# Performance work log

Measured on AMD Instinct MI355X. Metric: run time of the kernel, lower is better.

The kernel has to match this reference:

```python
import jax, jax.numpy as jnp
import numpy as np

B, S, H = 2, 2048, 2048
NH, NKV = 16, 4
DH = H // NH            # 128
I = 4 * H               # 8192
EPS = 1e-6


def rms_norm(x, w, eps=EPS):
    xf = x.astype(jnp.float32)
    var = jnp.mean(xf * xf, axis=-1, keepdims=True)
    return (w * (xf * jax.lax.rsqrt(var + eps))).astype(x.dtype)


def rotate_half(x):
    x1, x2 = jnp.split(x, 2, axis=-1)
    return jnp.concatenate([-x2, x1], axis=-1)


def setup_inputs() -> dict:
    key = jax.random.key(0)
    ks = jax.random.split(key, 12)
    hidden_states = jax.random.normal(ks[0], (B, S, H), jnp.float32)
    # rotary cos/sin over head_dim, standard RoPE table
    inv_freq = 1.0 / (10000.0 ** (np.arange(0, DH, 2, dtype=np.float32) / DH))
    t = np.arange(S, dtype=np.float32)
    freqs = np.einsum('i,j->ij', t, inv_freq)          # [S, DH/2]
    emb = np.concatenate([freqs, freqs], axis=-1)      # [S, DH]
    cos = jnp.broadcast_to(jnp.asarray(np.cos(emb))[None], (B, S, DH))
    sin = jnp.broadcast_to(jnp.asarray(np.sin(emb))[None], (B, S, DH))
    sd = lambda fan_in: 1.0 / np.sqrt(fan_in)
    return {
        'hidden_states': hidden_states,
        'cos': cos, 'sin': sin,
        'wq': jax.random.normal(ks[1], (H, NH * DH), jnp.float32) * sd(H),
        'wk': jax.random.normal(ks[2], (H, NKV * DH), jnp.float32) * sd(H),
        'wv': jax.random.normal(ks[3], (H, NKV * DH), jnp.float32) * sd(H),
        'wo': jax.random.normal(ks[4], (NH * DH, H), jnp.float32) * sd(H),
        'q_norm_w': jnp.ones((DH,), jnp.float32),
        'k_norm_w': jnp.ones((DH,), jnp.float32),
        'attn_norm_w': jnp.ones((H,), jnp.float32),
        'mlp_norm_w': jnp.ones((H,), jnp.float32),
        'w_gate': jax.random.normal(ks[5], (H, I), jnp.float32) * sd(H),
        'w_up': jax.random.normal(ks[6], (H, I), jnp.float32) * sd(H),
        'w_down': jax.random.normal(ks[7], (I, H), jnp.float32) * sd(I),
    }


def reference(hidden_states, cos, sin, wq, wk, wv, wo,
              q_norm_w, k_norm_w, attn_norm_w, mlp_norm_w,
              w_gate, w_up, w_down):
    b, s, _ = hidden_states.shape
    groups = NH // NKV
    scaling = DH ** -0.5

    # ---- attention sub-block ----
    residual = hidden_states
    x = rms_norm(hidden_states, attn_norm_w)

    q = (x @ wq).reshape(b, s, NH, DH)
    k = (x @ wk).reshape(b, s, NKV, DH)
    v = (x @ wv).reshape(b, s, NKV, DH)

    # per-head RMSNorm on head_dim (QK-norm)
    q = rms_norm(q, q_norm_w)
    k = rms_norm(k, k_norm_w)

    q = q.transpose(0, 2, 1, 3)  # [b, NH, s, DH]
    k = k.transpose(0, 2, 1, 3)  # [b, NKV, s, DH]
    v = v.transpose(0, 2, 1, 3)

    c = cos[:, None]  # [b, 1, s, DH]
    sn = sin[:, None]
    q = q * c + rotate_half(q) * sn
    k = k * c + rotate_half(k) * sn

    # GQA: fold query heads into [b, NKV, groups, s, DH]; avoid repeat_kv copy
    qg = q.reshape(b, NKV, groups, s, DH)
    scores = jnp.einsum('bkgqd,bkjd->bkgqj', qg, k) * scaling
    probs = jax.nn.softmax(scores.astype(jnp.float32), axis=-1).astype(hidden_states.dtype)
    attn = jnp.einsum('bkgqj,bkjd->bkgqd', probs, v)  # [b, NKV, groups, s, DH]
    attn = attn.reshape(b, NH, s, DH).transpose(0, 2, 1, 3).reshape(b, s, NH * DH)
    hidden_states = residual + attn @ wo

    # ---- SwiGLU MLP sub-block ----
    residual = hidden_states
    x = rms_norm(hidden_states, mlp_norm_w)
    h = jax.nn.silu(x @ w_gate) * (x @ w_up)
    hidden_states = residual + h @ w_down
    return hidden_states
```

## Files before the change

### kernel.cpp

```cpp
#include <hip/hip_runtime.h>
#include <stdint.h>

#define B_ 2
#define S_ 2048
#define H_ 2048
#define NH_ 16
#define NKV_ 4
#define DH_ 128
#define M_ (B_*S_)

typedef unsigned short u16;
typedef __attribute__((ext_vector_type(8))) short short8;
typedef __attribute__((ext_vector_type(4))) float floatx4;

__device__ __forceinline__ float b2f(u16 h) {
  union { unsigned int u; float f; } v; v.u = ((unsigned int)h) << 16; return v.f;
}
__device__ __forceinline__ u16 f2b(float f) {
  union { float f; unsigned int u; } v; v.f = f;
  unsigned int u = v.u;
  unsigned int r = (u + 0x7FFFu + ((u >> 16) & 1u)) >> 16;
  return (u16)r;
}
__device__ __forceinline__ floatx4 mfma16(short8 a, short8 b, floatx4 c) {
  return __builtin_amdgcn_mfma_f32_16x16x32_bf16(a, b, c, 0, 0, 0);
}
__device__ __forceinline__ void gld16(const u16* g, u16* l) {
  __builtin_amdgcn_global_load_lds(
      (const __attribute__((address_space(1))) unsigned int*)g,
      (__attribute__((address_space(3))) unsigned int*)l, 16, 0, 0);
}

__global__ __launch_bounds__(256) void transpose_kernel(const float* __restrict__ Bm,
                                                        u16* __restrict__ BT,
                                                        int K, int N) {
  __shared__ u16 sl[64][68];
  int t = threadIdx.x;
  int n0 = blockIdx.x * 64, k0 = blockIdx.y * 64;
#pragma unroll
  for (int p = 0; p < 4; ++p) {
    int kk = p * 16 + (t >> 4);
    int nn = (t & 15) * 4;
    float4 v = *(const float4*)&Bm[(size_t)(k0 + kk) * N + n0 + nn];
    sl[kk][nn + 0] = f2b(v.x); sl[kk][nn + 1] = f2b(v.y);
    sl[kk][nn + 2] = f2b(v.z); sl[kk][nn + 3] = f2b(v.w);
  }
  __syncthreads();
#pragma unroll
  for (int p = 0; p < 2; ++p) {
    int nn = p * 32 + (t >> 3);
    int kc = (t & 7) * 8;
    u16 ov[8];
#pragma unroll
    for (int j = 0; j < 8; ++j) ov[j] = sl[kc + j][nn];
    *(uint4*)&BT[(size_t)(n0 + nn) * K + k0 + kc] = *(uint4*)ov;
  }
}

__global__ __launch_bounds__(256) void rmsnorm_kernel(const float* __restrict__ x,
                                                      const float* __restrict__ w,
                                                      u16* __restrict__ o) {
  int row = blockIdx.x;
  int tid = threadIdx.x;
  const float* xr = x + (size_t)row * H_ + tid * 8;
  float4 a = *(const float4*)xr;
  float4 b = *(const float4*)(xr + 4);
  float xf[8] = {a.x, a.y, a.z, a.w, b.x, b.y, b.z, b.w};
  float ss = 0.f;
#pragma unroll
  for (int i = 0; i < 8; ++i) ss += xf[i] * xf[i];
#pragma unroll
  for (int m = 32; m >= 1; m >>= 1) ss += __shfl_xor(ss, m, 64);
  __shared__ float red[4];
  if ((tid & 63) == 0) red[tid >> 6] = ss;
  __syncthreads();
  float tot = red[0] + red[1] + red[2] + red[3];
  float scale = rsqrtf(tot / (float)H_ + 1e-6f);
  const float* wr = w + tid * 8;
  float4 wa = *(const float4*)wr;
  float4 wb = *(const float4*)(wr + 4);
  float wf[8] = {wa.x, wa.y, wa.z, wa.w, wb.x, wb.y, wb.z, wb.w};
  u16 ov[8];
#pragma unroll
  for (int i = 0; i < 8; ++i) ov[i] = f2b(xf[i] * scale * wf[i]);
  *(uint4*)&o[(size_t)row * H_ + tid * 8] = *(uint4*)ov;
}

template <int OUTF>
__global__ __launch_bounds__(256) void gemm_t(const u16* __restrict__ A,
                                              const u16* __restrict__ BT,
                                              void* __restrict__ Cv,
                                              const float* __restrict__ Res,
                                              int M, int N, int K) {
  __shared__ u16 sa[128 * 32];
  __shared__ u16 sb[128 * 32];
  const int tid = threadIdx.x;
  const int lane = tid & 63, w = tid >> 6;
  const int q4 = lane >> 4, l15 = lane & 15;
  const int wr = (w >> 1) * 64, wc = (w & 1) * 64;
  const int m0 = blockIdx.y * 128, n0 = blockIdx.x * 128;
  const int srow = lane >> 2, skc = (lane & 3) * 8;
  const int c0 = w * 2;
  floatx4 acc[4][4] = {};
  const u16* aG0 = A  + (size_t)(m0 + (c0 + 0) * 16 + srow) * K + skc;
  const u16* aG1 = A  + (size_t)(m0 + (c0 + 1) * 16 + srow) * K + skc;
  const u16* bG0 = BT + (size_t)(n0 + (c0 + 0) * 16 + srow) * K + skc;
  const u16* bG1 = BT + (size_t)(n0 + (c0 + 1) * 16 + srow) * K + skc;
  u16* aL0 = sa + (c0 + 0) * 512;
  u16* aL1 = sa + (c0 + 1) * 512;
  u16* bL0 = sb + (c0 + 0) * 512;
  u16* bL1 = sb + (c0 + 1) * 512;

  for (int k0 = 0; k0 < K; k0 += 32) {
    __syncthreads();
    gld16(aG0 + k0, aL0);
    gld16(aG1 + k0, aL1);
    gld16(bG0 + k0, bL0);
    gld16(bG1 + k0, bL1);
    __syncthreads();
    short8 af[4], bf[4];
#pragma unroll
    for (int i = 0; i < 4; ++i)
      af[i] = *(const short8*)&sa[(wr + i * 16 + l15) * 32 + q4 * 8];
#pragma unroll
    for (int j = 0; j < 4; ++j)
      bf[j] = *(const short8*)&sb[(wc + j * 16 + l15) * 32 + q4 * 8];
#pragma unroll
    for (int i = 0; i < 4; ++i)
#pragma unroll
      for (int j = 0; j < 4; ++j)
        acc[i][j] = mfma16(af[i], bf[j], acc[i][j]);
  }
#pragma unroll
  for (int i = 0; i < 4; ++i)
#pragma unroll
    for (int j = 0; j < 4; ++j)
#pragma unroll
      for (int r = 0; r < 4; ++r) {
        int row = m0 + wr + i * 16 + q4 * 4 + r;
        int col = n0 + wc + j * 16 + l15;
        float v = acc[i][j][r];
        if (OUTF) {
          if (Res) v += Res[(size_t)row * N + col];
          ((float*)Cv)[(size_t)row * N + col] = v;
        } else {
          ((u16*)Cv)[(size_t)row * N + col] = f2b(v);
        }
      }
}

__global__ __launch_bounds__(256) void gateup_kernel(const u16* __restrict__ A,
                                                     const u16* __restrict__ GT,
                                                     const u16* __restrict__ UT,
                                                     u16* __restrict__ O,
                                                     int M, int N, int K) {
  __shared__ u16 sa[128 * 32];
  __shared__ u16 sg[64 * 32];
  __shared__ u16 su[64 * 32];
  const int tid = threadIdx.x;
  const int lane = tid & 63, w = tid >> 6;
  const int q4 = lane >> 4, l15 = lane & 15;
  const int wr = (w >> 1) * 64, wc = (w & 1) * 32;
  const int m0 = blockIdx.y * 128, n0 = blockIdx.x * 64;
  const int srow = lane >> 2, skc = (lane & 3) * 8;
  const int c0 = w * 2;
  floatx4 accg[4][2] = {};
  floatx4 accu[4][2] = {};
  const u16* aG0 = A  + (size_t)(m0 + (c0 + 0) * 16 + srow) * K + skc;
  const u16* aG1 = A  + (size_t)(m0 + (c0 + 1) * 16 + srow) * K + skc;
  const u16* gG  = GT + (size_t)(n0 + w * 16 + srow) * K + skc;
  const u16* uG  = UT + (size_t)(n0 + w * 16 + srow) * K + skc;
  u16* aL0 = sa + (c0 + 0) * 512;
  u16* aL1 = sa + (c0 + 1) * 512;
  u16* gL  = sg + w * 512;
  u16* uL  = su + w * 512;

  for (int k0 = 0; k0 < K; k0 += 32) {
    __syncthreads();
    gld16(aG0 + k0, aL0);
    gld16(aG1 + k0, aL1);
    gld16(gG + k0, gL);
    gld16(uG + k0, uL);
    __syncthreads();
    short8 af[4], gf[2], uf[2];
#pragma unroll
    for (int i = 0; i < 4; ++i)
      af[i] = *(const short8*)&sa[(wr + i * 16 + l15) * 32 + q4 * 8];
#pragma unroll
    for (int j = 0; j < 2; ++j) {
      gf[j] = *(const short8*)&sg[(wc + j * 16 + l15) * 32 + q4 * 8];
      uf[j] = *(const short8*)&su[(wc + j * 16 + l15) * 32 + q4 * 8];
    }
#pragma unroll
    for (int i = 0; i < 4; ++i)
#pragma unroll
      for (int j = 0; j < 2; ++j) {
        accg[i][j] = mfma16(af[i], gf[j], accg[i][j]);
        accu[i][j] = mfma16(af[i], uf[j], accu[i][j]);
      }
  }
#pragma unroll
  for (int i = 0; i < 4; ++i)
#pragma unroll
    for (int j = 0; j < 2; ++j)
#pragma unroll
      for (int r = 0; r < 4; ++r) {
        int row = m0 + wr + i * 16 + q4 * 4 + r;
        int col = n0 + wc + j * 16 + l15;
        float g = accg[i][j][r];
        float u = accu[i][j][r];
        float s = g / (1.f + __expf(-g));
        O[(size_t)row * N + col] = f2b(s * u);
      }
}

__global__ __launch_bounds__(256) void qknorm_rope_kernel(u16* __restrict__ x,
                                                          const float* __restrict__ nw,
                                                          const float* __restrict__ cs,
                                                          const float* __restrict__ sn,
                                                          int nheads, int rowStride) {
  int lane = threadIdx.x & 63;
  int w = threadIdx.x >> 6;
  int gw = blockIdx.x * 4 + w;
  int t = gw / nheads, h = gw % nheads;
  u16* xp = x + (size_t)t * rowStride + h * DH_;
  float x0 = b2f(xp[lane]), x1 = b2f(xp[lane + 64]);
  float ss = x0 * x0 + x1 * x1;
#pragma unroll
  for (int m = 32; m >= 1; m >>= 1) ss += __shfl_xor(ss, m, 64);
  float scale = rsqrtf(ss / 128.f + 1e-6f);
  float n0 = x0 * scale * nw[lane];
  float n1 = x1 * scale * nw[lane + 64];
  const float* cp = cs + (size_t)t * DH_;
  const float* sp = sn + (size_t)t * DH_;
  float c0 = cp[lane], c1 = cp[lane + 64];
  float s0 = sp[lane], s1 = sp[lane + 64];
  xp[lane]      = f2b(n0 * c0 - n1 * s0);
  xp[lane + 64] = f2b(n1 * c1 + n0 * s1);
}

__global__ __launch_bounds__(256) void attn_kernel(const u16* __restrict__ qb,
                                                   const u16* __restrict__ kb,
                                                   const u16* __restrict__ vb,
                                                   u16* __restrict__ ob) {
  __shared__ u16 q_lds[64][136];
  __shared__ u16 k_lds[64][136];
  __shared__ u16 vt_lds[128][72];
  __shared__ u16 p_lds[4][16][72];
  const int QSTR = NH_ * DH_ + NKV_ * DH_ * 2;
  int tid = threadIdx.x;
  int lane = tid & 63, w = tid >> 6;
  int q4 = lane >> 4, l15 = lane & 15;
  int qt = blockIdx.x & 31;
  int h = (blockIdx.x >> 5) & 15;
  int b = blockIdx.x >> 9;
  int kvh = h >> 2;
  int srow = tid >> 2;
  int sd0 = (tid & 3) * 32;
  const float scaling = 0.08838834764831845f;

  {
    const u16* qsrc = qb + (size_t)(b * S_ + qt * 64 + srow) * QSTR + h * DH_;
#pragma unroll
    for (int ii = 0; ii < 4; ++ii) {
      int d = sd0 + ii * 8;
      *(uint4*)&q_lds[srow][d] = *(const uint4*)&qsrc[d];
    }
  }

  float m_i[4], l_i[4];
  floatx4 o_acc[8] = {};
#pragma unroll
  for (int r = 0; r < 4; ++r) { m_i[r] = -1e30f; l_i[r] = 0.f; }

  for (int c = 0; c < S_ / 64; ++c) {
    int j0 = c * 64;
    __syncthreads();
    const u16* ksrc = kb + (size_t)(b * S_ + j0 + srow) * QSTR + kvh * DH_;
    const u16* vsrc = vb + (size_t)(b * S_ + j0 + srow) * QSTR + kvh * DH_;
#pragma unroll
    for (int ii = 0; ii < 4; ++ii) {
      int d = sd0 + ii * 8;
      *(uint4*)&k_lds[srow][d] = *(const uint4*)&ksrc[d];
      uint4 vv = *(const uint4*)&vsrc[d];
      const u16* ve = (const u16*)&vv;
#pragma unroll
      for (int e = 0; e < 8; ++e) vt_lds[d + e][srow] = ve[e];
    }
    __syncthreads();

    floatx4 sc[4];
#pragma unroll
    for (int js = 0; js < 4; ++js) {
      floatx4 a = {};
#pragma unroll
      for (int kk = 0; kk < 4; ++kk) {
        short8 qa  = *(const short8*)&q_lds[w * 16 + l15][kk * 32 + q4 * 8];
        short8 kbf = *(const short8*)&k_lds[js * 16 + l15][kk * 32 + q4 * 8];
        a = mfma16(qa, kbf, a);
      }
      sc[js] = a;
    }
    float mx[4];
#pragma unroll
    for (int r = 0; r < 4; ++r)
      mx[r] = fmaxf(fmaxf(sc[0][r], sc[1][r]), fmaxf(sc[2][r], sc[3][r])) * scaling;
#pragma unroll
    for (int m = 8; m >= 1; m >>= 1)
#pragma unroll
      for (int r = 0; r < 4; ++r) mx[r] = fmaxf(mx[r], __shfl_xor(mx[r], m, 64));
    float alpha[4], rs[4];
#pragma unroll
    for (int r = 0; r < 4; ++r) {
      float mnew = fmaxf(m_i[r], mx[r]);
      alpha[r] = __expf(m_i[r] - mnew);
      m_i[r] = mnew;
      rs[r] = 0.f;
    }
#pragma unroll
    for (int js = 0; js < 4; ++js)
#pragma unroll
      for (int r = 0; r < 4; ++r) {
        float p = __expf(sc[js][r] * scaling - m_i[r]);
        rs[r] += p;
        p_lds[w][q4 * 4 + r][js * 16 + l15] = f2b(p);
      }
#pragma unroll
    for (int m = 8; m >= 1; m >>= 1)
#pragma unroll
      for (int r = 0; r < 4; ++r) rs[r] += __shfl_xor(rs[r], m, 64);
#pragma unroll
    for (int r = 0; r < 4; ++r) l_i[r] = l_i[r] * alpha[r] + rs[r];
#pragma unroll
    for (int d2 = 0; d2 < 8; ++d2)
#pragma unroll
      for (int r = 0; r < 4; ++r) o_acc[d2][r] *= alpha[r];
    __syncthreads();
#pragma unroll
    for (int d2 = 0; d2 < 8; ++d2) {
#pragma unroll
      for (int kk = 0; kk < 2; ++kk) {
        short8 pa  = *(const short8*)&p_lds[w][l15][kk * 32 + q4 * 8];
        short8 vbf = *(const short8*)&vt_lds[d2 * 16 + l15][kk * 32 + q4 * 8];
        o_acc[d2] = mfma16(pa, vbf, o_acc[d2]);
      }
    }
  }
#pragma unroll
  for (int d2 = 0; d2 < 8; ++d2)
#pragma unroll
    for (int r = 0; r < 4; ++r) {
      int row = qt * 64 + w * 16 + q4 * 4 + r;
      float val = o_acc[d2][r] / l_i[r];
      ob[(size_t)(b * S_ + row) * (NH_ * DH_) + h * DH_ + d2 * 16 + l15] = f2b(val);
    }
}

extern "C" void kernel_launch(void* const* d_in, const int* in_sizes, int n_in,
                              void* d_out, int out_size, void* d_ws, size_t ws_size,
                              hipStream_t stream) {
  const float* hs   = (const float*)d_in[0];
  const float* cosb = (const float*)d_in[1];
  const float* sinb = (const float*)d_in[2];
  const float* wq   = (const float*)d_in[3];
  const float* wk   = (const float*)d_in[4];
  const float* wv   = (const float*)d_in[5];
  const float* wo   = (const float*)d_in[6];
  const float* qnw  = (const float*)d_in[7];
  const float* knw  = (const float*)d_in[8];
  const float* anw  = (const float*)d_in[9];
  const float* mnw  = (const float*)d_in[10];
  const float* wg   = (const float*)d_in[11];
  const float* wu   = (const float*)d_in[12];
  const float* wd   = (const float*)d_in[13];
  float* out = (float*)d_out;
  u16* ws  = (u16*)d_ws;

  u16* wqkvT = ws;
  u16* woT   = ws + 6291456;
  u16* wgT   = ws + 10485760;
  u16* wuT   = ws + 27262976;
  u16* wdT   = ws + 44040192;
  u16* xn    = ws + 60817408;
  u16* qkv   = ws + 69206016;
  float* h1  = (float*)(ws + 81788928);
  u16* hbuf  = ws + 98566144;

  transpose_kernel<<<dim3(2048/64, 2048/64), 256, 0, stream>>>(wq, wqkvT, 2048, 2048);
  transpose_kernel<<<dim3(512/64,  2048/64), 256, 0, stream>>>(wk, wqkvT + (size_t)2048*2048, 2048, 512);
  transpose_kernel<<<dim3(512/64,  2048/64), 256, 0, stream>>>(wv, wqkvT + (size_t)2560*2048, 2048, 512);
  transpose_kernel<<<dim3(2048/64, 2048/64), 256, 0, stream>>>(wo, woT, 2048, 2048);
  transpose_kernel<<<dim3(8192/64, 2048/64), 256, 0, stream>>>(wg, wgT, 2048, 8192);
  transpose_kernel<<<dim3(8192/64, 2048/64), 256, 0, stream>>>(wu, wuT, 2048, 8192);
  transpose_kernel<<<dim3(2048/64, 8192/64), 256, 0, stream>>>(wd, wdT, 8192, 2048);

  rmsnorm_kernel<<<M_, 256, 0, stream>>>(hs, anw, xn);
  gemm_t<0><<<dim3(3072/128, M_/128), 256, 0, stream>>>(xn, wqkvT, qkv, nullptr, M_, 3072, 2048);
  qknorm_rope_kernel<<<M_ * NH_  / 4, 256, 0, stream>>>(qkv,        qnw, cosb, sinb, NH_,  3072);
  qknorm_rope_kernel<<<M_ * NKV_ / 4, 256, 0, stream>>>(qkv + 2048, knw, cosb, sinb, NKV_, 3072);
  attn_kernel<<<B_ * NH_ * (S_ / 64), 256, 0, stream>>>(qkv, qkv + 2048, qkv + 2560, xn);
  gemm_t<1><<<dim3(2048/128, M_/128), 256, 0, stream>>>(xn, woT, h1, hs, M_, 2048, 2048);
  u16* x2 = qkv;
  rmsnorm_kernel<<<M_, 256, 0, stream>>>(h1, mnw, x2);
  gateup_kernel<<<dim3(8192/64, M_/128), 256, 0, stream>>>(x2, wgT, wuT, hbuf, M_, 8192, 2048);
  gemm_t<1><<<dim3(2048/128, M_/128), 256, 0, stream>>>(hbuf, wdT, out, h1, M_, 2048, 8192);
}
```

Before: 1.280 ms.

## Replace GEMMs with 4-stage pipelined 256-row tile kernel with swizzled LDS

The simple single-buffered GEMM and fused gate/up kernel are replaced by one templated GEMM. It uses 512 threads, 256xBN tiles and a 4-deep LDS ring buffer with vmcnt-based waits, so global loads overlap MFMA work. LDS columns are XOR-swizzled to cut bank conflicts, and s_setprio is raised around the MFMA blocks. The gate/up fusion is split into two passes: up is written first as bf16, then the gate GEMM reads it back in its epilogue to apply SiLU. This adds an extra read and write of the intermediate plus a rounding of up to bf16 before the multiply. LDS use is much larger, which may limit occupancy.

Result: slower. 1.405 ms (+9.8%).

```diff
diff --git a/kernel.cpp b/kernel.cpp
--- a/kernel.cpp
+++ b/kernel.cpp
@@ -86,132 +86,102 @@
   *(uint4*)&o[(size_t)row * H_ + tid * 8] = *(uint4*)ov;
 }
 
-template <int OUTF>
-__global__ __launch_bounds__(256) void gemm_t(const u16* __restrict__ A,
+template <int BN, int OUTF>
+__global__ __launch_bounds__(512) void gemm_p(const u16* __restrict__ A,
                                               const u16* __restrict__ BT,
                                               void* __restrict__ Cv,
                                               const float* __restrict__ Res,
                                               int M, int N, int K) {
-  __shared__ u16 sa[128 * 32];
-  __shared__ u16 sb[128 * 32];
+  constexpr int WN    = (BN == 256) ? 4 : 2;
+  constexpr int WROWS = (BN == 256) ? 128 : 64;
+  constexpr int AFRAG = WROWS / 16;
+  constexpr int IPT   = 2 + BN / 128;
+  __shared__ __align__(16) u16 sa[4][256 * 32];
+  __shared__ __align__(16) u16 sb[4][BN * 32];
   const int tid = threadIdx.x;
   const int lane = tid & 63, w = tid >> 6;
   const int q4 = lane >> 4, l15 = lane & 15;
-  const int wr = (w >> 1) * 64, wc = (w & 1) * 64;
-  const int m0 = blockIdx.y * 128, n0 = blockIdx.x * 128;
-  const int srow = lane >> 2, skc = (lane & 3) * 8;
-  const int c0 = w * 2;
-  floatx4 acc[4][4] = {};
-  const u16* aG0 = A  + (size_t)(m0 + (c0 + 0) * 16 + srow) * K + skc;
-  const u16* aG1 = A  + (size_t)(m0 + (c0 + 1) * 16 + srow) * K + skc;
-  const u16* bG0 = BT + (size_t)(n0 + (c0 + 0) * 16 + srow) * K + skc;
-  const u16* bG1 = BT + (size_t)(n0 + (c0 + 1) * 16 + srow) * K + skc;
-  u16* aL0 = sa + (c0 + 0) * 512;
-  u16* aL1 = sa + (c0 + 1) * 512;
-  u16* bL0 = sb + (c0 + 0) * 512;
-  u16* bL1 = sb + (c0 + 1) * 512;
-
-  for (int k0 = 0; k0 < K; k0 += 32) {
-    __syncthreads();
-    gld16(aG0 + k0, aL0);
-    gld16(aG1 + k0, aL1);
-    gld16(bG0 + k0, bL0);
-    gld16(bG1 + k0, bL1);
-    __syncthreads();
-    short8 af[4], bf[4];
-#pragma unroll
-    for (int i = 0; i < 4; ++i)
-      af[i] = *(const short8*)&sa[(wr + i * 16 + l15) * 32 + q4 * 8];
+  const int wm = w / WN, wn = w % WN;
+  const int m0 = blockIdx.y * 256, n0 = blockIdx.x * BN;
+  const int srow = tid >> 2;
+  const int scb  = (tid & 3) ^ ((tid >> 3) & 3);
+  const u16* aS = A  + (size_t)(m0 + srow) * K + scb * 8;
+  const u16* bS = BT + (size_t)(n0 + srow) * K + scb * 8;
+  const int lOff = w * 512;
+  const int colSwz = (q4 ^ ((l15 >> 1) & 3)) * 8;
+  const int arow0 = wm * WROWS + l15;
+  const int brow0 = wn * 64 + l15;
+  const int NT = K / 32;
+  floatx4 acc[AFRAG][4] = {};
+
+  auto stage = [&](int tt) {
+    const int bb = tt & 3;
+    const int ko = tt * 32;
+    gld16(aS + ko,                   &sa[bb][lOff]);
+    gld16(aS + (size_t)128 * K + ko, &sa[bb][4096 + lOff]);
+    gld16(bS + ko,                   &sb[bb][lOff]);
+    if constexpr (BN == 256)
+      gld16(bS + (size_t)128 * K + ko, &sb[bb][4096 + lOff]);
+  };
+
+  stage(0); stage(1); stage(2);
+  for (int t = 0; t < NT; ++t) {
+    const u16* sab = sa[t & 3];
+    const u16* sbb = sb[t & 3];
+    const int left = NT - 1 - t;
+    if (left >= 2) {
+      asm volatile("s_waitcnt vmcnt(%0)" :: "n"(2 * IPT) : "memory");
+    } else if (left == 1) {
+      asm volatile("s_waitcnt vmcnt(%0)" :: "n"(IPT) : "memory");
+    } else {
+      asm volatile("s_waitcnt vmcnt(0)" ::: "memory");
+    }
+    __builtin_amdgcn_s_barrier();
+    asm volatile("" ::: "memory");
+    if (t + 3 < NT) stage(t + 3);
+    short8 bfr[4];
 #pragma unroll
     for (int j = 0; j < 4; ++j)
-      bf[j] = *(const short8*)&sb[(wc + j * 16 + l15) * 32 + q4 * 8];
-#pragma unroll
-    for (int i = 0; i < 4; ++i)
-#pragma unroll
-      for (int j = 0; j < 4; ++j)
-        acc[i][j] = mfma16(af[i], bf[j], acc[i][j]);
-  }
-#pragma unroll
-  for (int i = 0; i < 4; ++i)
-#pragma unroll
-    for (int j = 0; j < 4; ++j)
+      bfr[j] = *(const short8*)&sbb[(brow0 + j * 16) * 32 + colSwz];
+#pragma unroll
+    for (int ih = 0; ih < AFRAG / 4; ++ih) {
+      short8 afr[4];
+#pragma unroll
+      for (int i2 = 0; i2 < 4; ++i2)
+        afr[i2] = *(const short8*)&sab[(arow0 + (ih * 4 + i2) * 16) * 32 + colSwz];
+      __builtin_amdgcn_s_setprio(1);
+#pragma unroll
+      for (int i2 = 0; i2 < 4; ++i2)
+#pragma unroll
+        for (int j = 0; j < 4; ++j)
+          acc[ih * 4 + i2][j] = mfma16(afr[i2], bfr[j], acc[ih * 4 + i2][j]);
+      __builtin_amdgcn_s_setprio(0);
+    }
+  }
+
+#pragma unroll
+  for (int i = 0; i < AFRAG; ++i)
+#pragma unroll
+    for (int j = 0; j < 4; ++j) {
+      const int row0 = m0 + wm * WROWS + i * 16 + q4 * 4;
+      const int col  = n0 + wn * 64 + j * 16 + l15;
 #pragma unroll
       for (int r = 0; r < 4; ++r) {
-        int row = m0 + wr + i * 16 + q4 * 4 + r;
-        int col = n0 + wc + j * 16 + l15;
+        const size_t idx = (size_t)(row0 + r) * N + col;
         float v = acc[i][j][r];
-        if (OUTF) {
-          if (Res) v += Res[(size_t)row * N + col];
-          ((float*)Cv)[(size_t)row * N + col] = v;
+        if constexpr (OUTF == 1) {
+          if (Res) v += Res[idx];
+          ((float*)Cv)[idx] = v;
+        } else if constexpr (OUTF == 2) {
+          u16* O = (u16*)Cv;
+          float u = b2f(O[idx]);
+          float s = v / (1.f + __expf(-v));
+          O[idx] = f2b(s * u);
         } else {
-          ((u16*)Cv)[(size_t)row * N + col] = f2b(v);
+          ((u16*)Cv)[idx] = f2b(v);
         }
       }
-}
-
-__global__ __launch_bounds__(256) void gateup_kernel(const u16* __restrict__ A,
-                                                     const u16* __restrict__ GT,
-                                                     const u16* __restrict__ UT,
-                                                     u16* __restrict__ O,
-                                                     int M, int N, int K) {
-  __shared__ u16 sa[128 * 32];
-  __shared__ u16 sg[64 * 32];
-  __shared__ u16 su[64 * 32];
-  const int tid = threadIdx.x;
-  const int lane = tid & 63, w = tid >> 6;
-  const int q4 = lane >> 4, l15 = lane & 15;
-  const int wr = (w >> 1) * 64, wc = (w & 1) * 32;
-  const int m0 = blockIdx.y * 128, n0 = blockIdx.x * 64;
-  const int srow = lane >> 2, skc = (lane & 3) * 8;
-  const int c0 = w * 2;
-  floatx4 accg[4][2] = {};
-  floatx4 accu[4][2] = {};
-  const u16* aG0 = A  + (size_t)(m0 + (c0 + 0) * 16 + srow) * K + skc;
-  const u16* aG1 = A  + (size_t)(m0 + (c0 + 1) * 16 + srow) * K + skc;
-  const u16* gG  = GT + (size_t)(n0 + w * 16 + srow) * K + skc;
-  const u16* uG  = UT + (size_t)(n0 + w * 16 + srow) * K + skc;
-  u16* aL0 = sa + (c0 + 0) * 512;
-  u16* aL1 = sa + (c0 + 1) * 512;
-  u16* gL  = sg + w * 512;
-  u16* uL  = su + w * 512;
-
-  for (int k0 = 0; k0 < K; k0 += 32) {
-    __syncthreads();
-    gld16(aG0 + k0, aL0);
-    gld16(aG1 + k0, aL1);
-    gld16(gG + k0, gL);
-    gld16(uG + k0, uL);
-    __syncthreads();
-    short8 af[4], gf[2], uf[2];
-#pragma unroll
-    for (int i = 0; i < 4; ++i)
-      af[i] = *(const short8*)&sa[(wr + i * 16 + l15) * 32 + q4 * 8];
-#pragma unroll
-    for (int j = 0; j < 2; ++j) {
-      gf[j] = *(const short8*)&sg[(wc + j * 16 + l15) * 32 + q4 * 8];
-      uf[j] = *(const short8*)&su[(wc + j * 16 + l15) * 32 + q4 * 8];
-    }
-#pragma unroll
-    for (int i = 0; i < 4; ++i)
-#pragma unroll
-      for (int j = 0; j < 2; ++j) {
-        accg[i][j] = mfma16(af[i], gf[j], accg[i][j]);
-        accu[i][j] = mfma16(af[i], uf[j], accu[i][j]);
-      }
-  }
-#pragma unroll
-  for (int i = 0; i < 4; ++i)
-#pragma unroll
-    for (int j = 0; j < 2; ++j)
-#pragma unroll
-      for (int r = 0; r < 4; ++r) {
-        int row = m0 + wr + i * 16 + q4 * 4 + r;
-        int col = n0 + wc + j * 16 + l15;
-        float g = accg[i][j][r];
-        float u = accu[i][j][r];
-        float s = g / (1.f + __expf(-g));
-        O[(size_t)row * N + col] = f2b(s * u);
-      }
+    }
 }
 
 __global__ __launch_bounds__(256) void qknorm_rope_kernel(u16* __restrict__ x,
@@ -395,13 +365,14 @@
   transpose_kernel<<<dim3(2048/64, 8192/64), 256, 0, stream>>>(wd, wdT, 8192, 2048);
 
   rmsnorm_kernel<<<M_, 256, 0, stream>>>(hs, anw, xn);
-  gemm_t<0><<<dim3(3072/128, M_/128), 256, 0, stream>>>(xn, wqkvT, qkv, nullptr, M_, 3072, 2048);
+  gemm_p<256,0><<<dim3(3072/256, M_/256), 512, 0, stream>>>(xn, wqkvT, qkv, nullptr, M_, 3072, 2048);
   qknorm_rope_kernel<<<M_ * NH_  / 4, 256, 0, stream>>>(qkv,        qnw, cosb, sinb, NH_,  3072);
   qknorm_rope_kernel<<<M_ * NKV_ / 4, 256, 0, stream>>>(qkv + 2048, knw, cosb, sinb, NKV_, 3072);
   attn_kernel<<<B_ * NH_ * (S_ / 64), 256, 0, stream>>>(qkv, qkv + 2048, qkv + 2560, xn);
-  gemm_t<1><<<dim3(2048/128, M_/128), 256, 0, stream>>>(xn, woT, h1, hs, M_, 2048, 2048);
+  gemm_p<128,1><<<dim3(2048/128, M_/256), 512, 0, stream>>>(xn, woT, h1, hs, M_, 2048, 2048);
   u16* x2 = qkv;
   rmsnorm_kernel<<<M_, 256, 0, stream>>>(h1, mnw, x2);
-  gateup_kernel<<<dim3(8192/64, M_/128), 256, 0, stream>>>(x2, wgT, wuT, hbuf, M_, 8192, 2048);
-  gemm_t<1><<<dim3(2048/128, M_/128), 256, 0, stream>>>(hbuf, wdT, out, h1, M_, 2048, 8192);
-}
+  gemm_p<256,0><<<dim3(8192/256, M_/256), 512, 0, stream>>>(x2, wuT, hbuf, nullptr, M_, 8192, 2048);
+  gemm_p<256,2><<<dim3(8192/256, M_/256), 512, 0, stream>>>(x2, wgT, hbuf, nullptr, M_, 8192, 2048);
+  gemm_p<128,1><<<dim3(2048/128, M_/256), 512, 0, stream>>>(hbuf, wdT, out, h1, M_, 2048, 8192);
+}
```

## Add 256x256 pipelined GEMM with interleaved gate/up weights for QKV and MLP

Applied to the files above, without the earlier changes.

Adds a new 512-thread GEMM kernel with 256x256 tiles, a double-buffered LDS pipeline using direct global-to-LDS loads, XOR-swizzled LDS layout, explicit barriers and waitcnts, priority hints, and XCD-aware block remapping. Gate and up weights are transposed into one interleaved matrix in 128-column blocks, so a single GEMM produces both, and the SwiGLU is applied in the epilogue by exchanging the up half through LDS. The new kernel replaces both the QKV projection and the old gate/up kernel. It relies on hand-placed synchronization and register pressure at occupancy 2, and the up values are rounded to bf16 before the multiply.

Measured after the change: 1.244 ms. -2.8%, faster.

```diff
diff --git a/kernel.cpp b/kernel.cpp
--- a/kernel.cpp
+++ b/kernel.cpp
@@ -31,9 +31,16 @@
       (__attribute__((address_space(3))) unsigned int*)l, 16, 0, 0);
 }
 
+#define BAR()    asm volatile("s_barrier" ::: "memory")
+#define LGKM0()  asm volatile("s_waitcnt lgkmcnt(0)" ::: "memory")
+#define VMC(n)   asm volatile("s_waitcnt vmcnt(" #n ")" ::: "memory")
+#define SCHEDB() __builtin_amdgcn_sched_barrier(0)
+#define PRIO1()  __builtin_amdgcn_s_setprio(1)
+#define PRIO0()  __builtin_amdgcn_s_setprio(0)
+
 __global__ __launch_bounds__(256) void transpose_kernel(const float* __restrict__ Bm,
                                                         u16* __restrict__ BT,
-                                                        int K, int N) {
+                                                        int K, int N, int ileave) {
   __shared__ u16 sl[64][68];
   int t = threadIdx.x;
   int n0 = blockIdx.x * 64, k0 = blockIdx.y * 64;
@@ -53,7 +60,10 @@
     u16 ov[8];
 #pragma unroll
     for (int j = 0; j < 8; ++j) ov[j] = sl[kc + j][nn];
-    *(uint4*)&BT[(size_t)(n0 + nn) * K + k0 + kc] = *(uint4*)ov;
+    int n = n0 + nn;
+    int n_out = n;
+    if (ileave) n_out = ((n >> 7) << 8) + ((ileave == 2) ? 128 : 0) + (n & 127);
+    *(uint4*)&BT[(size_t)n_out * K + k0 + kc] = *(uint4*)ov;
   }
 }
 
@@ -149,69 +159,189 @@
       }
 }
 
-__global__ __launch_bounds__(256) void gateup_kernel(const u16* __restrict__ A,
-                                                     const u16* __restrict__ GT,
-                                                     const u16* __restrict__ UT,
-                                                     u16* __restrict__ O,
-                                                     int M, int N, int K) {
-  __shared__ u16 sa[128 * 32];
-  __shared__ u16 sg[64 * 32];
-  __shared__ u16 su[64 * 32];
+template <int OUTF>
+__global__ __launch_bounds__(512, 2) void gemm8(const u16* __restrict__ A,
+                                                const u16* __restrict__ BT,
+                                                void* __restrict__ Cv,
+                                                int M, int N, int K,
+                                                int gm, int ldO) {
+  __shared__ u16 sA[2][2][8192];
+  __shared__ u16 sB[2][2][8192];
   const int tid = threadIdx.x;
   const int lane = tid & 63, w = tid >> 6;
   const int q4 = lane >> 4, l15 = lane & 15;
-  const int wr = (w >> 1) * 64, wc = (w & 1) * 32;
-  const int m0 = blockIdx.y * 128, n0 = blockIdx.x * 64;
-  const int srow = lane >> 2, skc = (lane & 3) * 8;
-  const int c0 = w * 2;
-  floatx4 accg[4][2] = {};
-  floatx4 accu[4][2] = {};
-  const u16* aG0 = A  + (size_t)(m0 + (c0 + 0) * 16 + srow) * K + skc;
-  const u16* aG1 = A  + (size_t)(m0 + (c0 + 1) * 16 + srow) * K + skc;
-  const u16* gG  = GT + (size_t)(n0 + w * 16 + srow) * K + skc;
-  const u16* uG  = UT + (size_t)(n0 + w * 16 + srow) * K + skc;
-  u16* aL0 = sa + (c0 + 0) * 512;
-  u16* aL1 = sa + (c0 + 1) * 512;
-  u16* gL  = sg + w * 512;
-  u16* uL  = su + w * 512;
-
-  for (int k0 = 0; k0 < K; k0 += 32) {
-    __syncthreads();
-    gld16(aG0 + k0, aL0);
-    gld16(aG1 + k0, aL1);
-    gld16(gG + k0, gL);
-    gld16(uG + k0, uL);
-    __syncthreads();
-    short8 af[4], gf[2], uf[2];
+  const int wm = w >> 2, wn = w & 3;
+  const int nwg = gridDim.x;
+  const int qx = nwg >> 3, rx = nwg & 7;
+  const int xcd = blockIdx.x & 7, idxx = blockIdx.x >> 3;
+  const int wgid = (xcd < rx ? xcd * (qx + 1) : rx * (qx + 1) + (xcd - rx) * qx) + idxx;
+  const int m0 = (wgid % gm) * 256, n0 = (wgid / gm) * 256;
+
+  const int sr = tid >> 3;
+  const int sblk = ((tid & 7) ^ (sr & 7)) << 3;
+  const u16* aS = A  + (size_t)(m0 + sr) * K + sblk;
+  const u16* bS = BT + (size_t)(n0 + sr) * K + sblk;
+  const size_t K64 = (size_t)K << 6;
+  const int wofs = w * 512;
+
+  const int cA  = (q4 ^ (l15 & 7)) << 3;
+  const int bh  = wn >> 1;
+  const int bb  = (wn & 1) * 64;
+  const int NT  = K >> 6;
+
+  floatx4 acc[8][4] = {};
+
+  auto stA = [&](int c, int k0) {
+    const u16* s0 = aS + k0;
+    gld16(s0,            &sA[c][0][wofs]);
+    gld16(s0 + K64,      &sA[c][0][4096 + wofs]);
+    gld16(s0 + 2 * K64,  &sA[c][1][wofs]);
+    gld16(s0 + 3 * K64,  &sA[c][1][4096 + wofs]);
+  };
+  auto stB = [&](int c, int k0) {
+    const u16* s0 = bS + k0;
+    gld16(s0,            &sB[c][0][wofs]);
+    gld16(s0 + K64,      &sB[c][0][4096 + wofs]);
+    gld16(s0 + 2 * K64,  &sB[c][1][wofs]);
+    gld16(s0 + 3 * K64,  &sB[c][1][4096 + wofs]);
+  };
+
+  stB(0, 0); stA(0, 0);
+  stB(1, 64); stA(1, 64);
+  VMC(8);
+  BAR();
+
+  short8 aR[4][2], bR[4][2];
+#pragma unroll 1
+  for (int t = 0; t < NT; ++t) {
+    const int c = t & 1;
+    const u16* aH = &sA[c][wm][0];
+    const u16* bH = &sB[c][bh][0];
+    const bool pf = (t + 2 < NT);
+    const int kp = (t + 2) << 6;
+
+#pragma unroll
+    for (int i = 0; i < 4; ++i) {
+      const int ro = (i * 16 + l15) * 64;
+      aR[i][0] = *(const short8*)&aH[ro + cA];
+      aR[i][1] = *(const short8*)&aH[ro + (cA ^ 32)];
+    }
+#pragma unroll
+    for (int j = 0; j < 2; ++j) {
+      const int ro = (bb + j * 16 + l15) * 64;
+      bR[j][0] = *(const short8*)&bH[ro + cA];
+      bR[j][1] = *(const short8*)&bH[ro + (cA ^ 32)];
+    }
+    BAR(); LGKM0(); SCHEDB();
+    PRIO1();
 #pragma unroll
     for (int i = 0; i < 4; ++i)
-      af[i] = *(const short8*)&sa[(wr + i * 16 + l15) * 32 + q4 * 8];
-#pragma unroll
-    for (int j = 0; j < 2; ++j) {
-      gf[j] = *(const short8*)&sg[(wc + j * 16 + l15) * 32 + q4 * 8];
-      uf[j] = *(const short8*)&su[(wc + j * 16 + l15) * 32 + q4 * 8];
-    }
+#pragma unroll
+      for (int j = 0; j < 2; ++j) {
+        acc[i][j] = mfma16(aR[i][0], bR[j][0], acc[i][j]);
+        acc[i][j] = mfma16(aR[i][1], bR[j][1], acc[i][j]);
+      }
+    PRIO0();
+    BAR();
+
+#pragma unroll
+    for (int j = 2; j < 4; ++j) {
+      const int ro = (bb + j * 16 + l15) * 64;
+      bR[j][0] = *(const short8*)&bH[ro + cA];
+      bR[j][1] = *(const short8*)&bH[ro + (cA ^ 32)];
+    }
+    BAR(); LGKM0(); SCHEDB();
+    PRIO1();
 #pragma unroll
     for (int i = 0; i < 4; ++i)
 #pragma unroll
+      for (int j = 2; j < 4; ++j) {
+        acc[i][j] = mfma16(aR[i][0], bR[j][0], acc[i][j]);
+        acc[i][j] = mfma16(aR[i][1], bR[j][1], acc[i][j]);
+      }
+    PRIO0();
+    BAR();
+
+#pragma unroll
+    for (int i = 0; i < 4; ++i) {
+      const int ro = ((i + 4) * 16 + l15) * 64;
+      aR[i][0] = *(const short8*)&aH[ro + cA];
+      aR[i][1] = *(const short8*)&aH[ro + (cA ^ 32)];
+    }
+    if (pf) stB(c, kp);
+    BAR(); LGKM0(); SCHEDB();
+    PRIO1();
+#pragma unroll
+    for (int i = 0; i < 4; ++i)
+#pragma unroll
+      for (int j = 2; j < 4; ++j) {
+        acc[i + 4][j] = mfma16(aR[i][0], bR[j][0], acc[i + 4][j]);
+        acc[i + 4][j] = mfma16(aR[i][1], bR[j][1], acc[i + 4][j]);
+      }
+    PRIO0();
+    BAR();
+
+    if (pf) stA(c, kp);
+    if (pf) { VMC(8); }
+    else if (t + 1 < NT) { VMC(0); }
+    BAR(); SCHEDB();
+    PRIO1();
+#pragma unroll
+    for (int i = 0; i < 4; ++i)
+#pragma unroll
       for (int j = 0; j < 2; ++j) {
-        accg[i][j] = mfma16(af[i], gf[j], accg[i][j]);
-        accu[i][j] = mfma16(af[i], uf[j], accu[i][j]);
-      }
-  }
-#pragma unroll
-  for (int i = 0; i < 4; ++i)
-#pragma unroll
-    for (int j = 0; j < 2; ++j)
-#pragma unroll
-      for (int r = 0; r < 4; ++r) {
-        int row = m0 + wr + i * 16 + q4 * 4 + r;
-        int col = n0 + wc + j * 16 + l15;
-        float g = accg[i][j][r];
-        float u = accu[i][j][r];
-        float s = g / (1.f + __expf(-g));
-        O[(size_t)row * N + col] = f2b(s * u);
-      }
+        acc[i + 4][j] = mfma16(aR[i][0], bR[j][0], acc[i + 4][j]);
+        acc[i + 4][j] = mfma16(aR[i][1], bR[j][1], acc[i + 4][j]);
+      }
+    PRIO0();
+    BAR();
+  }
+
+  if constexpr (OUTF == 0) {
+#pragma unroll
+    for (int i = 0; i < 8; ++i)
+#pragma unroll
+      for (int j = 0; j < 4; ++j)
+#pragma unroll
+        for (int r = 0; r < 4; ++r) {
+          const int row = m0 + wm * 128 + i * 16 + q4 * 4 + r;
+          const int col = n0 + wn * 64 + j * 16 + l15;
+          ((u16*)Cv)[(size_t)row * ldO + col] = f2b(acc[i][j][r]);
+        }
+  } else {
+    u16* X = &sA[0][0][0];
+    __syncthreads();
+    if (wn >= 2) {
+#pragma unroll
+      for (int i = 0; i < 8; ++i)
+#pragma unroll
+        for (int j = 0; j < 4; ++j)
+#pragma unroll
+          for (int r = 0; r < 4; ++r) {
+            const int rl = i * 16 + q4 * 4 + r;
+            const int uc = (wn - 2) * 64 + j * 16 + l15;
+            X[(size_t)(wm * 128 + rl) * 128 + uc] = f2b(acc[i][j][r]);
+          }
+    }
+    __syncthreads();
+    if (wn < 2) {
+#pragma unroll
+      for (int i = 0; i < 8; ++i)
+#pragma unroll
+        for (int j = 0; j < 4; ++j)
+#pragma unroll
+          for (int r = 0; r < 4; ++r) {
+            const int rl = i * 16 + q4 * 4 + r;
+            const int gc = wn * 64 + j * 16 + l15;
+            float g = acc[i][j][r];
+            float u = b2f(X[(size_t)(wm * 128 + rl) * 128 + gc]);
+            float s = g / (1.f + __expf(-g));
+            const int row = m0 + wm * 128 + rl;
+            const int ocol = (n0 >> 1) + gc;
+            ((u16*)Cv)[(size_t)row * ldO + ocol] = f2b(s * u);
+          }
+    }
+  }
 }
 
 __global__ __launch_bounds__(256) void qknorm_rope_kernel(u16* __restrict__ x,
@@ -378,30 +508,29 @@
 
   u16* wqkvT = ws;
   u16* woT   = ws + 6291456;
-  u16* wgT   = ws + 10485760;
-  u16* wuT   = ws + 27262976;
+  u16* wguT  = ws + 10485760;
   u16* wdT   = ws + 44040192;
   u16* xn    = ws + 60817408;
   u16* qkv   = ws + 69206016;
   float* h1  = (float*)(ws + 81788928);
   u16* hbuf  = ws + 98566144;
 
-  transpose_kernel<<<dim3(2048/64, 2048/64), 256, 0, stream>>>(wq, wqkvT, 2048, 2048);
-  transpose_kernel<<<dim3(512/64,  2048/64), 256, 0, stream>>>(wk, wqkvT + (size_t)2048*2048, 2048, 512);
-  transpose_kernel<<<dim3(512/64,  2048/64), 256, 0, stream>>>(wv, wqkvT + (size_t)2560*2048, 2048, 512);
-  transpose_kernel<<<dim3(2048/64, 2048/64), 256, 0, stream>>>(wo, woT, 2048, 2048);
-  transpose_kernel<<<dim3(8192/64, 2048/64), 256, 0, stream>>>(wg, wgT, 2048, 8192);
-  transpose_kernel<<<dim3(8192/64, 2048/64), 256, 0, stream>>>(wu, wuT, 2048, 8192);
-  transpose_kernel<<<dim3(2048/64, 8192/64), 256, 0, stream>>>(wd, wdT, 8192, 2048);
+  transpose_kernel<<<dim3(2048/64, 2048/64), 256, 0, stream>>>(wq, wqkvT, 2048, 2048, 0);
+  transpose_kernel<<<dim3(512/64,  2048/64), 256, 0, stream>>>(wk, wqkvT + (size_t)2048*2048, 2048, 512, 0);
+  transpose_kernel<<<dim3(512/64,  2048/64), 256, 0, stream>>>(wv, wqkvT + (size_t)2560*2048, 2048, 512, 0);
+  transpose_kernel<<<dim3(2048/64, 2048/64), 256, 0, stream>>>(wo, woT, 2048, 2048, 0);
+  transpose_kernel<<<dim3(8192/64, 2048/64), 256, 0, stream>>>(wg, wguT, 2048, 8192, 1);
+  transpose_kernel<<<dim3(8192/64, 2048/64), 256, 0, stream>>>(wu, wguT, 2048, 8192, 2);
+  transpose_kernel<<<dim3(2048/64, 8192/64), 256, 0, stream>>>(wd, wdT, 8192, 2048, 0);
 
   rmsnorm_kernel<<<M_, 256, 0, stream>>>(hs, anw, xn);
-  gemm_t<0><<<dim3(3072/128, M_/128), 256, 0, stream>>>(xn, wqkvT, qkv, nullptr, M_, 3072, 2048);
+  gemm8<0><<<16 * 12, 512, 0, stream>>>(xn, wqkvT, qkv, M_, 3072, 2048, 16, 3072);
   qknorm_rope_kernel<<<M_ * NH_  / 4, 256, 0, stream>>>(qkv,        qnw, cosb, sinb, NH_,  3072);
   qknorm_rope_kernel<<<M_ * NKV_ / 4, 256, 0, stream>>>(qkv + 2048, knw, cosb, sinb, NKV_, 3072);
   attn_kernel<<<B_ * NH_ * (S_ / 64), 256, 0, stream>>>(qkv, qkv + 2048, qkv + 2560, xn);
   gemm_t<1><<<dim3(2048/128, M_/128), 256, 0, stream>>>(xn, woT, h1, hs, M_, 2048, 2048);
   u16* x2 = qkv;
   rmsnorm_kernel<<<M_, 256, 0, stream>>>(h1, mnw, x2);
-  gateup_kernel<<<dim3(8192/64, M_/128), 256, 0, stream>>>(x2, wgT, wuT, hbuf, M_, 8192, 2048);
+  gemm8<3><<<16 * 64, 512, 0, stream>>>(x2, wguT, hbuf, M_, 16384, 2048, 16, 8192);
   gemm_t<1><<<dim3(2048/128, M_/128), 256, 0, stream>>>(hbuf, wdT, out, h1, M_, 2048, 8192);
 }
```
